# Kernel tuning notes

Measured on AMD Instinct MI355X. Metric: run time of the kernel, lower is better.

Reference implementation:

```python
import jax, jax.numpy as jnp
import numpy as np

H, DR, DN = 16, 64, 64
HD = DR + DN  # 128
EPS = 1e-6


def _ln(t):
    m = t.mean(-1, keepdims=True)
    v = ((t - m) ** 2).mean(-1, keepdims=True)
    return (t - m) / jnp.sqrt(v + EPS)


def _rms(t, w):
    return t * jax.lax.rsqrt((t * t).mean(-1, keepdims=True) + EPS) * w


def _rot(t, fcs):
    # t: [b,s,h,DR]; fcs: [s, DR//2, 2] (cos,sin); complex multiply on pairs
    b, s, h, d = t.shape
    tr = t.reshape(b, s, h, d // 2, 2)
    x0, x1 = tr[..., 0], tr[..., 1]
    cos = fcs[None, :, None, :, 0]
    sin = fcs[None, :, None, :, 1]
    o0 = x0 * cos - x1 * sin
    o1 = x0 * sin + x1 * cos
    return jnp.stack([o0, o1], axis=-1).reshape(b, s, h, d)


def setup_inputs() -> dict:
    key = jax.random.key(0)
    ks = jax.random.split(key, 12)
    B, SX, SY, D = 1, 2048, 512, 2048
    s = 0.02
    pos_x = jnp.arange(SX, dtype=jnp.float32)
    pos_y = jnp.arange(SY, dtype=jnp.float32)
    inv = 1.0 / (10000.0 ** (jnp.arange(0, DR, 2, dtype=jnp.float32) / DR))  # [32]
    ang_x = pos_x[:, None] * inv[None, :]
    ang_y = pos_y[:, None] * inv[None, :]
    return {
        "x": jax.random.normal(ks[0], (B, SX, D), jnp.float32),
        "y": jax.random.normal(ks[1], (B, SY, D), jnp.float32),
        "mod": jax.random.normal(ks[2], (B, D), jnp.float32),
        "freqs_x": jnp.stack([jnp.cos(ang_x), jnp.sin(ang_x)], -1),
        "freqs_y": jnp.stack([jnp.cos(ang_y), jnp.sin(ang_y)], -1),
        "mask_x": jnp.ones((B, SX), bool),
        "mask_y": jnp.ones((B, SY), bool),
        "Wqkv_x": jax.random.normal(ks[3], (HD * H * 3, D), jnp.float32) * s,
        "bqkv_x": jnp.zeros((HD * H * 3,), jnp.float32),
        "Wqkv_y": jax.random.normal(ks[4], (HD * H * 3, D), jnp.float32) * s,
        "bqkv_y": jnp.zeros((HD * H * 3,), jnp.float32),
        "Wout": jax.random.normal(ks[5], (D, HD * H), jnp.float32) * s,
        "bout": jnp.zeros((D,), jnp.float32),
        "wq": jnp.ones((HD,), jnp.float32),
        "wk": jnp.ones((HD,), jnp.float32),
        "Wmod_q": jax.random.normal(ks[6], (D * 3, D), jnp.float32) * s,
        "bmod_q": jnp.zeros((D * 3,), jnp.float32),
        "Wmod_kv": jax.random.normal(ks[7], (D * 3, D), jnp.float32) * s,
        "bmod_kv": jnp.zeros((D * 3,), jnp.float32),
    }


def reference(x, y, mod, freqs_x, freqs_y, mask_x, mask_y, Wqkv_x, bqkv_x,
              Wqkv_y, bqkv_y, Wout, bout, wq, wk, Wmod_q, bmod_q, Wmod_kv, bmod_kv):
    b, sx, D = x.shape
    sy = y.shape[1]
    sz = sx + sy
    x_res, y_res = x, y
    xn = _ln(x)
    yn = _ln(y)
    # modulation from mod vector [b, D] -> [b, 1, 3D]
    mq = mod[:, None, :] @ Wmod_q.T + bmod_q
    bias_x, scale_x, gate_x = jnp.split(mq, 3, axis=-1)
    mkv = mod[:, None, :] @ Wmod_kv.T + bmod_kv
    bias_y, scale_y, gate_y = jnp.split(mkv, 3, axis=-1)
    xm = (1.0 + scale_x) * xn + bias_x
    ym = (1.0 + scale_y) * yn + bias_y
    qx, kx, vx = jnp.split(xm @ Wqkv_x.T + bqkv_x, 3, axis=-1)
    qy, ky, vy = jnp.split(ym @ Wqkv_y.T + bqkv_y, 3, axis=-1)
    q = jnp.concatenate([qx, qy], 1).reshape(b, sz, H, HD)
    k = jnp.concatenate([kx, ky], 1).reshape(b, sz, H, HD)
    v = jnp.concatenate([vx, vy], 1).reshape(b, sz, H, HD)
    q = _rms(q, wq)
    k = _rms(k, wk)
    q_rope, q_nope = q[..., :DR], q[..., DR:]
    k_rope, k_nope = k[..., :DR], k[..., DR:]
    fxx = jnp.concatenate([freqs_x, jnp.zeros_like(freqs_y)], 0)
    fyy = jnp.concatenate([jnp.zeros_like(freqs_x), freqs_y], 0)
    qf = jnp.concatenate([_rot(q_rope, fxx), _rot(q_rope, fyy), q_nope], -1)
    kf = jnp.concatenate([_rot(k_rope, fxx), _rot(k_rope, fyy), k_nope], -1)
    d_attn = 2 * DR + DN  # 192
    scale = 1.0 / jnp.sqrt(jnp.float32(d_attn))
    scores = jnp.einsum('bshd,bthd->bhst', qf, kf) * scale
    mask = jnp.concatenate([mask_x, mask_y], 1)  # [b, sz] bool, key-side
    scores = jnp.where(mask[:, None, None, :], scores, -jnp.inf)
    attn = jax.nn.softmax(scores, axis=-1)
    z = jnp.einsum('bhst,bthd->bshd', attn, v).reshape(b, sz, H * HD)
    z = z @ Wout.T + bout
    xo = z[:, :sx] * gate_x + x_res
    yo = z[:, sx:] * gate_y + y_res
    return jnp.concatenate([xo, yo], axis=1)  # [b, sz, D]
```

## Files before the change

kernel.cpp:

```cpp
#include <hip/hip_runtime.h>
#include <math.h>

#define H_    16
#define DR_   64
#define HD_   128
#define D_    2048
#define SX_   2048
#define SY_   512
#define SZ_   2560
#define NQKV_ 6144
#define EPS_  1e-6f
#define ATTN_SCALE 0.07216878364870323f
#define NS_   4
#define SPL_  (SZ_ / NS_)
#define QT_   (SZ_ / 128)

typedef __attribute__((ext_vector_type(8)))  short short8;
typedef __attribute__((ext_vector_type(16))) float f32x16;

__device__ __forceinline__ unsigned short f2bf(float f) {
    unsigned u = __builtin_bit_cast(unsigned, f);
    u += 0x7FFF + ((u >> 16) & 1);
    return (unsigned short)(u >> 16);
}
__device__ __forceinline__ unsigned pack2(float a, float b) {
    return (unsigned)f2bf(a) | ((unsigned)f2bf(b) << 16);
}
__device__ __forceinline__ float bf2f_lo(unsigned u) {
    return __builtin_bit_cast(float, u << 16);
}
__device__ __forceinline__ float bf2f_hi(unsigned u) {
    return __builtin_bit_cast(float, u & 0xffff0000u);
}

__device__ __forceinline__ unsigned cvtpk_bf16(float lo, float hi) {
    unsigned r;
    asm volatile("v_cvt_pk_bf16_f32 %0, %1, %2" : "=v"(r) : "v"(lo), "v"(hi));
    return r;
}

__device__ __forceinline__ void gload16(const unsigned short* g, unsigned short* l) {
    __builtin_amdgcn_global_load_lds(
        (const __attribute__((address_space(1))) unsigned*)g,
        (__attribute__((address_space(3))) unsigned*)l, 16, 0, 0);
}

__device__ __forceinline__ int xcd_swz(int hw, int nwg) {
    return (hw & 7) * (nwg >> 3) + (hw >> 3);
}

__device__ __forceinline__ short8 mkfrag(const float* p) {
    unsigned a01 = cvtpk_bf16(p[0], p[1]);
    unsigned a23 = cvtpk_bf16(p[2], p[3]);
    unsigned a45 = cvtpk_bf16(p[4], p[5]);
    unsigned a67 = cvtpk_bf16(p[6], p[7]);
    asm volatile("v_permlane32_swap_b32 %0, %1" : "+v"(a01), "+v"(a45));
    asm volatile("v_permlane32_swap_b32 %0, %1" : "+v"(a23), "+v"(a67));
    union { unsigned u[4]; short8 s; } r;
    r.u[0] = a01; r.u[1] = a23; r.u[2] = a45; r.u[3] = a67;
    return r.s;
}

__global__ __launch_bounds__(256) void cvt_all_kernel(
    const float* __restrict__ s1, const float* __restrict__ s2, const float* __restrict__ s3,
    unsigned short* __restrict__ dst, int n1, int n2, int n3)
{
    int i = (blockIdx.x * 256 + threadIdx.x) * 8;
    if (i >= n1 + n2 + n3) return;
    const float* src;
    if (i < n1)            src = s1 + i;
    else if (i < n1 + n2)  src = s2 + (i - n1);
    else                   src = s3 + (i - n1 - n2);
    float4 a = *(const float4*)(src);
    float4 b = *(const float4*)(src + 4);
    uint4 pk;
    pk.x = pack2(a.x, a.y); pk.y = pack2(a.z, a.w);
    pk.z = pack2(b.x, b.y); pk.w = pack2(b.z, b.w);
    *(uint4*)(dst + i) = pk;
}

__global__ __launch_bounds__(256) void mod_gemv_kernel(
    const float* __restrict__ mod,
    const float* __restrict__ Wq, const float* __restrict__ bq,
    const float* __restrict__ Wkv, const float* __restrict__ bkv,
    float* __restrict__ mq, float* __restrict__ mkv)
{
    int t = threadIdx.x;
    int row = blockIdx.x * 4 + (t >> 6);
    int lane = t & 63;
    const float* W; const float* b; float* out; int r;
    if (row < NQKV_) { W = Wq;  b = bq;  out = mq;  r = row; }
    else             { W = Wkv; b = bkv; out = mkv; r = row - NQKV_; }
    const float* wr = W + (size_t)r * D_;
    float s = 0.f;
    for (int k = lane; k < D_; k += 64) s += wr[k] * mod[k];
#pragma unroll
    for (int m = 32; m >= 1; m >>= 1) s += __shfl_xor(s, m);
    if (lane == 0) out[r] = s + b[r];
}

__global__ __launch_bounds__(256) void ln_mod_kernel(
    const float* __restrict__ x, const float* __restrict__ y,
    const float* __restrict__ mq, const float* __restrict__ mkv,
    unsigned short* __restrict__ xm)
{
    __shared__ float red[8];
    int s = blockIdx.x, t = threadIdx.x;
    const float* src; const float* mv;
    if (s < SX_) { src = x + (size_t)s * D_;          mv = mq; }
    else         { src = y + (size_t)(s - SX_) * D_;  mv = mkv; }
    float a[8];
    *(float4*)&a[0] = *(const float4*)(src + t * 8);
    *(float4*)&a[4] = *(const float4*)(src + t * 8 + 4);
    float sum = 0.f, ssq = 0.f;
#pragma unroll
    for (int i = 0; i < 8; ++i) { sum += a[i]; ssq += a[i] * a[i]; }
#pragma unroll
    for (int m = 32; m >= 1; m >>= 1) { sum += __shfl_xor(sum, m); ssq += __shfl_xor(ssq, m); }
    if ((t & 63) == 0) { red[t >> 6] = sum; red[4 + (t >> 6)] = ssq; }
    __syncthreads();
    float tot  = red[0] + red[1] + red[2] + red[3];
    float totq = red[4] + red[5] + red[6] + red[7];
    float mean = tot * (1.f / (float)D_);
    float var  = totq * (1.f / (float)D_) - mean * mean;
    float inv  = rsqrtf(var + EPS_);
    float o[8];
#pragma unroll
    for (int i = 0; i < 8; ++i) {
        int c = t * 8 + i;
        float v = (a[i] - mean) * inv;
        o[i] = (1.f + mv[D_ + c]) * v + mv[c];
    }
    uint4 pk;
    pk.x = pack2(o[0], o[1]); pk.y = pack2(o[2], o[3]);
    pk.z = pack2(o[4], o[5]); pk.w = pack2(o[6], o[7]);
    *(uint4*)(xm + (size_t)s * D_ + t * 8) = pk;
}

__global__ __launch_bounds__(256) void gemm_bf16_kernel(
    const unsigned short* __restrict__ A,
    const unsigned short* __restrict__ Wx, const float* __restrict__ bx,
    const unsigned short* __restrict__ Wy, const float* __restrict__ by,
    void* __restrict__ Cout, int N,
    const float* __restrict__ gx, const float* __restrict__ gy,
    const float* __restrict__ rx, const float* __restrict__ ry,
    int mode)
{
    __shared__ __align__(16) unsigned short As[2][128 * 32];
    __shared__ __align__(16) unsigned short Bs[2][128 * 32];
    int m0 = blockIdx.y * 128, n0 = blockIdx.x * 128;
    const unsigned short* W = (m0 < SX_) ? Wx : Wy;
    const float* bb = (m0 < SX_) ? bx : by;
    int t = threadIdx.x;
    int wv = t >> 6, lane = t & 63, l31 = lane & 31, g = lane >> 5;
    int wr = wv >> 1, wc = wv & 1;
    int srow = t >> 2, ssl = t & 3;
    const unsigned short* gA = A + (size_t)(m0 + srow) * D_ + ((ssl ^ ((srow >> 1) & 3)) * 8);
    const unsigned short* gW = W + (size_t)(n0 + srow) * D_ + ((ssl ^ ((srow >> 1) & 3)) * 8);
    f32x16 acc[2][2];
#pragma unroll
    for (int i = 0; i < 2; ++i)
#pragma unroll
        for (int j = 0; j < 2; ++j)
#pragma unroll
            for (int r = 0; r < 16; ++r) acc[i][j][r] = 0.f;
    int arow = wr * 64 + l31;
    int wrow = wc * 64 + l31;
    int a3 = (arow >> 1) & 3, w3 = (wrow >> 1) & 3;

    gload16(gA,            &As[0][wv * 512]);
    gload16(gA + 64 * D_,  &As[0][2048 + wv * 512]);
    gload16(gW,            &Bs[0][wv * 512]);
    gload16(gW + 64 * D_,  &Bs[0][2048 + wv * 512]);
    __syncthreads();

    for (int k0 = 0; k0 < D_; k0 += 32) {
        int cur = (k0 >> 5) & 1;
        if (k0 + 32 < D_) {
            int nb = cur ^ 1;
            gload16(gA + k0 + 32,           &As[nb][wv * 512]);
            gload16(gA + 64 * D_ + k0 + 32, &As[nb][2048 + wv * 512]);
            gload16(gW + k0 + 32,           &Bs[nb][wv * 512]);
            gload16(gW + 64 * D_ + k0 + 32, &Bs[nb][2048 + wv * 512]);
        }
#pragma unroll
        for (int kk = 0; kk < 2; ++kk) {
            int slot = kk * 2 + g;
            short8 af[2], wf[2];
#pragma unroll
            for (int i = 0; i < 2; ++i) {
                af[i] = *(const short8*)&As[cur][(arow + i * 32) * 32 + ((slot ^ a3) * 8)];
                wf[i] = *(const short8*)&Bs[cur][(wrow + i * 32) * 32 + ((slot ^ w3) * 8)];
            }
#pragma unroll
            for (int i = 0; i < 2; ++i)
#pragma unroll
                for (int j = 0; j < 2; ++j)
                    acc[i][j] = __builtin_amdgcn_mfma_f32_32x32x16_bf16(wf[j], af[i], acc[i][j], 0, 0, 0);
        }
        __syncthreads();
    }

#pragma unroll
    for (int i = 0; i < 2; ++i) {
        int row = m0 + wr * 64 + i * 32 + l31;
        if (mode == 0) {
            unsigned short* C = (unsigned short*)Cout;
#pragma unroll
            for (int j = 0; j < 2; ++j)
#pragma unroll
                for (int q = 0; q < 4; ++q) {
                    int n = n0 + wc * 64 + j * 32 + q * 8 + 4 * g;
                    float o0 = acc[i][j][q * 4 + 0] + bb[n + 0];
                    float o1 = acc[i][j][q * 4 + 1] + bb[n + 1];
                    float o2 = acc[i][j][q * 4 + 2] + bb[n + 2];
                    float o3 = acc[i][j][q * 4 + 3] + bb[n + 3];
                    *(uint2*)(C + (size_t)row * N + n) = make_uint2(pack2(o0, o1), pack2(o2, o3));
                }
        } else {
            float* C = (float*)Cout;
            const float* gt = (row < SX_) ? gx : gy;
            const float* rr = (row < SX_) ? rx + (size_t)row * N : ry + (size_t)(row - SX_) * N;
#pragma unroll
            for (int j = 0; j < 2; ++j)
#pragma unroll
                for (int q = 0; q < 4; ++q) {
                    int n = n0 + wc * 64 + j * 32 + q * 8 + 4 * g;
                    float4 o;
                    o.x = (acc[i][j][q * 4 + 0] + bb[n + 0]) * gt[n + 0] + rr[n + 0];
                    o.y = (acc[i][j][q * 4 + 1] + bb[n + 1]) * gt[n + 1] + rr[n + 1];
                    o.z = (acc[i][j][q * 4 + 2] + bb[n + 2]) * gt[n + 2] + rr[n + 2];
                    o.w = (acc[i][j][q * 4 + 3] + bb[n + 3]) * gt[n + 3] + rr[n + 3];
                    *(float4*)(C + (size_t)row * N + n) = o;
                }
        }
    }
}

__global__ __launch_bounds__(256) void qkv_transform_kernel(
    const unsigned short* __restrict__ qkv,
    const float* __restrict__ fx, const float* __restrict__ fy,
    const float* __restrict__ wq, const float* __restrict__ wk,
    unsigned short* __restrict__ qh, unsigned short* __restrict__ kh)
{
    int t = threadIdx.x;
    int gid = blockIdx.x * 4 + (t >> 6);
    int lane = t & 63;
    int s = gid >> 4;
    int h = gid & 15;
    const unsigned short* base = qkv + (size_t)s * NQKV_ + h * HD_;
    int d = lane * 2;
    unsigned qu = *(const unsigned*)(base + d);
    unsigned ku = *(const unsigned*)(base + 2048 + d);
    float qx = bf2f_lo(qu), qy = bf2f_hi(qu);
    float kx = bf2f_lo(ku), ky = bf2f_hi(ku);
    float sq = qx * qx + qy * qy;
    float sk = kx * kx + ky * ky;
#pragma unroll
    for (int m = 32; m >= 1; m >>= 1) { sq += __shfl_xor(sq, m); sk += __shfl_xor(sk, m); }
    float qs = rsqrtf(sq * (1.f / 128.f) + EPS_) * ATTN_SCALE;
    float ks = rsqrtf(sk * (1.f / 128.f) + EPS_);
    float q0 = qx * qs * wq[d], q1 = qy * qs * wq[d + 1];
    float k0 = kx * ks * wk[d], k1 = ky * ks * wk[d + 1];
    if (lane < 32) {
        const float* f = (s < SX_) ? fx + (size_t)s * DR_ + d
                                   : fy + (size_t)(s - SX_) * DR_ + d;
        float cs = f[0], sn = f[1];
        float o0 = q0 * cs - q1 * sn, o1 = q0 * sn + q1 * cs;
        q0 = o0; q1 = o1;
        o0 = k0 * cs - k1 * sn; o1 = k0 * sn + k1 * cs;
        k0 = o0; k1 = o1;
    }
    size_t off = ((size_t)h * SZ_ + s) * HD_ + d;
    *(unsigned*)(qh + off) = pack2(q0, q1);
    *(unsigned*)(kh + off) = pack2(k0, k1);
}

__global__ __launch_bounds__(256) void vtrans_kernel(
    const unsigned short* __restrict__ qkvb, unsigned short* __restrict__ vt)
{
    __shared__ __align__(16) unsigned short T[64][72];
    int h = blockIdx.z, d0 = blockIdx.y * 64, s0 = blockIdx.x * 64;
    int t = threadIdx.x;
    int r = t >> 2, c = (t & 3) * 16;
    const unsigned short* src = qkvb + (size_t)(s0 + r) * NQKV_ + 4096 + h * HD_ + d0 + c;
    *(short8*)&T[r][c]     = *(const short8*)(src);
    *(short8*)&T[r][c + 8] = *(const short8*)(src + 8);
    __syncthreads();
    unsigned short o16[16];
#pragma unroll
    for (int i = 0; i < 16; ++i) o16[i] = T[c + i][r];
    unsigned short* dst = vt + ((size_t)h * HD_ + d0 + r) * SZ_ + s0 + c;
    *(short8*)dst       = *(short8*)&o16[0];
    *(short8*)(dst + 8) = *(short8*)&o16[8];
}

__global__ __launch_bounds__(256) void attn_mfma_kernel(
    const unsigned short* __restrict__ qh, const unsigned short* __restrict__ kh,
    const unsigned short* __restrict__ vt,
    unsigned short* __restrict__ Opart, float* __restrict__ mpart, float* __restrict__ lpart)
{
    __shared__ __align__(16) short Ks[2][64 * 128];
    __shared__ __align__(16) short Vs[2][128 * 64];
    int hw = (blockIdx.z * gridDim.y + blockIdx.y) * gridDim.x + blockIdx.x;
    int lg = xcd_swz(hw, QT_ * H_ * NS_);
    int qt    = lg % QT_;
    int hs    = lg / QT_;
    int h     = hs % H_;
    int split = hs / H_;
    int t = threadIdx.x;
    int wv = t >> 6, lane = t & 63;
    int l31 = lane & 31, g = lane >> 5;
    int bq = qt * 128 + wv * 32;
    const unsigned short* kbase = kh + (size_t)h * SZ_ * HD_;
    const unsigned short* vbase = vt + (size_t)h * HD_ * SZ_;

    int koff[4], voff[4];
#pragma unroll
    for (int i = 0; i < 4; ++i) {
        int idx = i * 256 + t;
        int r = idx >> 4, sl = idx & 15;
        koff[i] = r * HD_ + (((sl & 8) | ((sl ^ (r & 7)) & 7)) * 8);
        int r2 = idx >> 3, sl2 = idx & 7;
        voff[i] = r2 * SZ_ + ((sl2 ^ (r2 & 7)) * 8);
    }
    int ldsOff = wv * 512;

    short8 qf[8];
    {
        const unsigned short* qb = qh + ((size_t)h * SZ_ + bq + l31) * HD_ + g * 8;
#pragma unroll
        for (int s = 0; s < 8; ++s) qf[s] = *(const short8*)(qb + s * 16);
    }

    f32x16 o[4];
#pragma unroll
    for (int db = 0; db < 4; ++db)
#pragma unroll
        for (int r = 0; r < 16; ++r) o[db][r] = 0.f;
    float mreg = -INFINITY, lreg = 0.f;
    bool qY = (bq >= SX_);
    int sw7 = l31 & 7;
    int ts0 = split * SPL_;
    const int NT = SPL_ / 64;

#pragma unroll
    for (int i = 0; i < 4; ++i)
        gload16(kbase + (size_t)ts0 * HD_ + koff[i], (unsigned short*)&Ks[0][0] + i * 2048 + ldsOff);
#pragma unroll
    for (int i = 0; i < 4; ++i)
        gload16(vbase + ts0 + voff[i], (unsigned short*)&Vs[0][0] + i * 2048 + ldsOff);
    __syncthreads();

    for (int it = 0; it < NT; ++it) {
        int t0 = ts0 + it * 64;
        int cur = it & 1;
        if (it + 1 < NT) {
            int nb = cur ^ 1;
            const unsigned short* kn = kbase + (size_t)(t0 + 64) * HD_;
            const unsigned short* vn = vbase + (t0 + 64);
#pragma unroll
            for (int i = 0; i < 4; ++i)
                gload16(kn + koff[i], (unsigned short*)&Ks[nb][0] + i * 2048 + ldsOff);
#pragma unroll
            for (int i = 0; i < 4; ++i)
                gload16(vn + voff[i], (unsigned short*)&Vs[nb][0] + i * 2048 + ldsOff);
        }

        bool same = (qY == (t0 >= SX_));
        f32x16 sc0, sc1;
#pragma unroll
        for (int r = 0; r < 16; ++r) { sc0[r] = 0.f; sc1[r] = 0.f; }
        const short* Krow0 = &Ks[cur][0] + l31 * 128;
        const short* Krow1 = &Ks[cur][0] + (l31 + 32) * 128;
        __builtin_amdgcn_s_setprio(1);
#pragma unroll
        for (int s = 4; s < 8; ++s) {
            int slot = 2 * s + g;
            int sl = (slot & 8) | ((slot ^ sw7) & 7);
            sc0 = __builtin_amdgcn_mfma_f32_32x32x16_bf16(*(const short8*)(Krow0 + sl * 8), qf[s], sc0, 0, 0, 0);
            sc1 = __builtin_amdgcn_mfma_f32_32x32x16_bf16(*(const short8*)(Krow1 + sl * 8), qf[s], sc1, 0, 0, 0);
        }
        if (same) {
#pragma unroll
            for (int s = 0; s < 4; ++s) {
                int slot = 2 * s + g;
                int sl = (slot & 8) | ((slot ^ sw7) & 7);
                sc0 = __builtin_amdgcn_mfma_f32_32x32x16_bf16(*(const short8*)(Krow0 + sl * 8), qf[s], sc0, 0, 0, 0);
                sc1 = __builtin_amdgcn_mfma_f32_32x32x16_bf16(*(const short8*)(Krow1 + sl * 8), qf[s], sc1, 0, 0, 0);
            }
        }
        __builtin_amdgcn_s_setprio(0);

        float pm = -INFINITY;
#pragma unroll
        for (int r = 0; r < 16; ++r) pm = fmaxf(pm, fmaxf(sc0[r], sc1[r]));
        pm = fmaxf(pm, __shfl_xor(pm, 32));
        float mnew = fmaxf(mreg, pm);
        float corr = __expf(mreg - mnew);
        mreg = mnew;
        float pp0[16], pp1[16]; float rs = 0.f;
#pragma unroll
        for (int r = 0; r < 16; ++r) {
            pp0[r] = __expf(sc0[r] - mnew);
            pp1[r] = __expf(sc1[r] - mnew);
            rs += pp0[r] + pp1[r];
        }
        rs += __shfl_xor(rs, 32);
        lreg = lreg * corr + rs;
#pragma unroll
        for (int db = 0; db < 4; ++db)
#pragma unroll
            for (int r = 0; r < 16; ++r) o[db][r] *= corr;

        short8 pa0 = mkfrag(&pp0[0]), pa1 = mkfrag(&pp0[8]);
        short8 pa2 = mkfrag(&pp1[0]), pa3 = mkfrag(&pp1[8]);
        const short* Vb = &Vs[cur][0];
        __builtin_amdgcn_s_setprio(1);
#pragma unroll
        for (int ks = 0; ks < 4; ++ks) {
            short8 pf = (ks == 0) ? pa0 : (ks == 1) ? pa1 : (ks == 2) ? pa2 : pa3;
#pragma unroll
            for (int db = 0; db < 4; ++db) {
                int row = db * 32 + l31;
                int sl = (2 * ks + g) ^ (l31 & 7);
                const short8 vf = *(const short8*)(Vb + row * 64 + sl * 8);
                o[db] = __builtin_amdgcn_mfma_f32_32x32x16_bf16(vf, pf, o[db], 0, 0, 0);
            }
        }
        __builtin_amdgcn_s_setprio(0);
        __syncthreads();
    }

    int basep = ((split * QT_ + qt) * H_ + h) * 128 + wv * 32 + l31;
    unsigned short* op = Opart + (size_t)basep * 128;
#pragma unroll
    for (int db = 0; db < 4; ++db)
#pragma unroll
        for (int r = 0; r < 16; ++r) {
            int d = db * 32 + (r & 3) + 8 * (r >> 2) + 4 * g;
            op[d] = f2bf(o[db][r]);
        }
    if (g == 0) { mpart[basep] = mreg; lpart[basep] = lreg; }
}

__global__ __launch_bounds__(256) void attn_combine_kernel(
    const unsigned short* __restrict__ Opart,
    const float* __restrict__ mpart, const float* __restrict__ lpart,
    unsigned short* __restrict__ z)
{
    int t = threadIdx.x;
    int gid = blockIdx.x * 4 + (t >> 6);
    int lane = t & 63;
    int h = gid & 15;
    int r = gid >> 4;
    int qtile = r >> 7, qi = r & 127;
    int pidx[NS_];
    float m[NS_];
    float mx = -INFINITY;
#pragma unroll
    for (int s = 0; s < NS_; ++s) {
        pidx[s] = ((s * QT_ + qtile) * H_ + h) * 128 + qi;
        m[s] = mpart[pidx[s]];
        mx = fmaxf(mx, m[s]);
    }
    float L = 0.f;
    float w[NS_];
#pragma unroll
    for (int s = 0; s < NS_; ++s) {
        w[s] = __expf(m[s] - mx);
        L += w[s] * lpart[pidx[s]];
    }
    float invL = 1.f / L;
    int d = lane * 2;
    float a0 = 0.f, a1 = 0.f;
#pragma unroll
    for (int s = 0; s < NS_; ++s) {
        unsigned u = *(const unsigned*)(Opart + (size_t)pidx[s] * 128 + d);
        a0 += w[s] * bf2f_lo(u);
        a1 += w[s] * bf2f_hi(u);
    }
    *(unsigned*)(z + (size_t)r * D_ + h * HD_ + d) = pack2(a0 * invL, a1 * invL);
}

extern "C" void kernel_launch(void* const* d_in, const int* in_sizes, int n_in,
                              void* d_out, int out_size, void* d_ws, size_t ws_size,
                              hipStream_t stream) {
    const float* x    = (const float*)d_in[0];
    const float* y    = (const float*)d_in[1];
    const float* mod  = (const float*)d_in[2];
    const float* fx   = (const float*)d_in[3];
    const float* fy   = (const float*)d_in[4];
    const float* Wqx  = (const float*)d_in[7];
    const float* bqx  = (const float*)d_in[8];
    const float* Wqy  = (const float*)d_in[9];
    const float* bqy  = (const float*)d_in[10];
    const float* Wout = (const float*)d_in[11];
    const float* bout = (const float*)d_in[12];
    const float* wq   = (const float*)d_in[13];
    const float* wk   = (const float*)d_in[14];
    const float* Wmq  = (const float*)d_in[15];
    const float* bmq  = (const float*)d_in[16];
    const float* Wmk  = (const float*)d_in[17];
    const float* bmk  = (const float*)d_in[18];

    float* mq   = (float*)d_ws;
    float* mkv  = mq + NQKV_;
    unsigned short* xm   = (unsigned short*)(mkv + NQKV_);
    unsigned short* qkvb = xm + (size_t)SZ_ * D_;
    unsigned short* qh   = qkvb + (size_t)SZ_ * NQKV_;
    unsigned short* kh   = qh + (size_t)H_ * SZ_ * HD_;
    unsigned short* vh   = kh + (size_t)H_ * SZ_ * HD_;
    unsigned short* vt   = vh + (size_t)H_ * SZ_ * HD_;
    unsigned short* wqxb = vt + (size_t)H_ * SZ_ * HD_;
    unsigned short* wqyb = wqxb + (size_t)NQKV_ * D_;
    unsigned short* wob  = wqyb + (size_t)NQKV_ * D_;
    unsigned short* z    = xm;
    unsigned short* Opart = wqxb;
    float* mpart = (float*)qkvb;
    float* lpart = mpart + NS_ * QT_ * H_ * 128;
    float* out  = (float*)d_out;

    const int n1 = NQKV_ * D_, n3 = D_ * D_;
    hipLaunchKernelGGL(cvt_all_kernel, dim3((2 * n1 + n3) / 2048), dim3(256), 0, stream,
                       Wqx, Wqy, Wout, wqxb, n1, n1, n3);
    hipLaunchKernelGGL(mod_gemv_kernel, dim3(2 * NQKV_ / 4), dim3(256), 0, stream,
                       mod, Wmq, bmq, Wmk, bmk, mq, mkv);
    hipLaunchKernelGGL(ln_mod_kernel, dim3(SZ_), dim3(256), 0, stream,
                       x, y, mq, mkv, xm);
    hipLaunchKernelGGL(gemm_bf16_kernel, dim3(NQKV_ / 128, SZ_ / 128), dim3(256), 0, stream,
                       xm, wqxb, bqx, wqyb, bqy, (void*)qkvb, NQKV_,
                       (const float*)nullptr, (const float*)nullptr,
                       (const float*)nullptr, (const float*)nullptr, 0);
    hipLaunchKernelGGL(qkv_transform_kernel, dim3(SZ_ * H_ / 4), dim3(256), 0, stream,
                       qkvb, fx, fy, wq, wk, qh, kh);
    hipLaunchKernelGGL(vtrans_kernel, dim3(SZ_ / 64, HD_ / 64, H_), dim3(256), 0, stream,
                       qkvb, vt);
    hipLaunchKernelGGL(attn_mfma_kernel, dim3(QT_, H_, NS_), dim3(256), 0, stream,
                       qh, kh, vt, Opart, mpart, lpart);
    hipLaunchKernelGGL(attn_combine_kernel, dim3(SZ_ * H_ / 4), dim3(256), 0, stream,
                       Opart, mpart, lpart, z);
    hipLaunchKernelGGL(gemm_bf16_kernel, dim3(D_ / 128, SZ_ / 128), dim3(256), 0, stream,
                       z, wob, bout, wob, bout, (void*)out, D_,
                       mq + 2 * D_, mkv + 2 * D_, x, y, 1);
}
```

Measured before the change: 344.4 us.

## Use a 256x256-tile, 512-thread GEMM kernel for the QKV projection

Adds a dedicated GEMM kernel for the QKV projection. It uses 256x256 output tiles, a K-step of 64, 8 waves each computing a 128x64 sub-tile with 32x32x16 bf16 MFMAs, and double-buffered swizzled LDS. The goal is more data reuse per byte loaded and fewer blocks than the previous 128x128 kernel. The cost is about 128KB of LDS per block, so only one block fits per CU, and a grid of 240 blocks that leaves some CUs idle.

After: 324.9 us. -5.6%, faster.

```diff
diff --git a/kernel.cpp b/kernel.cpp
--- a/kernel.cpp
+++ b/kernel.cpp
@@ -135,6 +135,92 @@
     pk.x = pack2(o[0], o[1]); pk.y = pack2(o[2], o[3]);
     pk.z = pack2(o[4], o[5]); pk.w = pack2(o[6], o[7]);
     *(uint4*)(xm + (size_t)s * D_ + t * 8) = pk;
+}
+
+__global__ __launch_bounds__(512, 2) void gemm8_bf16_kernel(
+    const unsigned short* __restrict__ A,
+    const unsigned short* __restrict__ Wx, const float* __restrict__ bx,
+    const unsigned short* __restrict__ Wy, const float* __restrict__ by,
+    unsigned short* __restrict__ C, int N)
+{
+    __shared__ __align__(16) unsigned short As[2][256 * 64];
+    __shared__ __align__(16) unsigned short Bs[2][256 * 64];
+    int m0 = blockIdx.y * 256, n0 = blockIdx.x * 256;
+    const unsigned short* W = (m0 < SX_) ? Wx : Wy;
+    const float* bb = (m0 < SX_) ? bx : by;
+    int t = threadIdx.x;
+    int wv = t >> 6, lane = t & 63, l31 = lane & 31, g = lane >> 5;
+    int wr = wv >> 2, wc = wv & 3;
+    int off[4];
+#pragma unroll
+    for (int i = 0; i < 4; ++i) {
+        int c = i * 512 + t, r = c >> 3, sl = c & 7;
+        off[i] = r * D_ + ((sl ^ (r & 7)) * 8);
+    }
+    const unsigned short* gA = A + (size_t)m0 * D_;
+    const unsigned short* gW = W + (size_t)n0 * D_;
+    int dstw = wv * 512;
+    f32x16 acc[4][2];
+#pragma unroll
+    for (int i = 0; i < 4; ++i)
+#pragma unroll
+        for (int j = 0; j < 2; ++j)
+#pragma unroll
+            for (int r = 0; r < 16; ++r) acc[i][j][r] = 0.f;
+    int arow = wr * 128 + l31;
+    int brow = wc * 64 + l31;
+    int s7 = l31 & 7;
+
+#pragma unroll
+    for (int i = 0; i < 4; ++i) gload16(gA + off[i], &As[0][i * 4096 + dstw]);
+#pragma unroll
+    for (int i = 0; i < 4; ++i) gload16(gW + off[i], &Bs[0][i * 4096 + dstw]);
+
+    const int NT = D_ / 64;
+    for (int kt = 0; kt < NT; ++kt) {
+        int cur = kt & 1;
+        asm volatile("s_waitcnt vmcnt(0)" ::: "memory");
+        __builtin_amdgcn_s_barrier();
+        if (kt + 1 < NT) {
+            int nb = cur ^ 1, k1 = (kt + 1) * 64;
+#pragma unroll
+            for (int i = 0; i < 4; ++i) gload16(gA + k1 + off[i], &As[nb][i * 4096 + dstw]);
+#pragma unroll
+            for (int i = 0; i < 4; ++i) gload16(gW + k1 + off[i], &Bs[nb][i * 4096 + dstw]);
+        }
+#pragma unroll
+        for (int ks = 0; ks < 4; ++ks) {
+            int sx = ((ks * 2 + g) ^ s7) * 8;
+            short8 af[4], bf[2];
+#pragma unroll
+            for (int i = 0; i < 4; ++i)
+                af[i] = *(const short8*)&As[cur][(arow + i * 32) * 64 + sx];
+#pragma unroll
+            for (int j = 0; j < 2; ++j)
+                bf[j] = *(const short8*)&Bs[cur][(brow + j * 32) * 64 + sx];
+#pragma unroll
+            for (int i = 0; i < 4; ++i)
+#pragma unroll
+                for (int j = 0; j < 2; ++j)
+                    acc[i][j] = __builtin_amdgcn_mfma_f32_32x32x16_bf16(bf[j], af[i], acc[i][j], 0, 0, 0);
+        }
+    }
+
+#pragma unroll
+    for (int i = 0; i < 4; ++i) {
+        int row = m0 + wr * 128 + i * 32 + l31;
+#pragma unroll
+        for (int j = 0; j < 2; ++j)
+#pragma unroll
+            for (int q = 0; q < 4; ++q) {
+                int n = n0 + wc * 64 + j * 32 + q * 8 + 4 * g;
+                float o0 = acc[i][j][q * 4 + 0] + bb[n + 0];
+                float o1 = acc[i][j][q * 4 + 1] + bb[n + 1];
+                float o2 = acc[i][j][q * 4 + 2] + bb[n + 2];
+                float o3 = acc[i][j][q * 4 + 3] + bb[n + 3];
+                *(uint2*)(C + (size_t)row * N + n) = make_uint2(pack2(o0, o1), pack2(o2, o3));
+            }
+    }
 }
 
 __global__ __launch_bounds__(256) void gemm_bf16_kernel(
@@ -528,10 +614,8 @@
                        mod, Wmq, bmq, Wmk, bmk, mq, mkv);
     hipLaunchKernelGGL(ln_mod_kernel, dim3(SZ_), dim3(256), 0, stream,
                        x, y, mq, mkv, xm);
-    hipLaunchKernelGGL(gemm_bf16_kernel, dim3(NQKV_ / 128, SZ_ / 128), dim3(256), 0, stream,
-                       xm, wqxb, bqx, wqyb, bqy, (void*)qkvb, NQKV_,
-                       (const float*)nullptr, (const float*)nullptr,
-                       (const float*)nullptr, (const float*)nullptr, 0);
+    hipLaunchKernelGGL(gemm8_bf16_kernel, dim3(NQKV_ / 256, SZ_ / 256), dim3(512), 0, stream,
+                       xm, wqxb, bqx, wqyb, bqy, qkvb, NQKV_);
     hipLaunchKernelGGL(qkv_transform_kernel, dim3(SZ_ * H_ / 4), dim3(256), 0, stream,
                        qkvb, fx, fy, wq, wk, qh, kh);
     hipLaunchKernelGGL(vtrans_kernel, dim3(SZ_ / 64, HD_ / 64, H_), dim3(256), 0, stream,
```
